# Optimization experiments

Hardware: AMD Instinct MI355X
Metric: run time of the kernel (lower is better)

The kernel has to match this reference:

```python
import jax, jax.numpy as jnp
import numpy as np

D = 256      # d_model (module-level constant in source)
H = 4        # num_heads
HD = D // H  # head dim = 64
B = 16
T = 512
STEP = 0.5   # self.step_size
NEG = -1e9
SCALE = 1.0 / np.sqrt(HD).astype(np.float32)


def _ln(x, g, b):
    m = jnp.mean(x, -1, keepdims=True)
    v = jnp.var(x, -1, keepdims=True)
    return (x - m) / jnp.sqrt(v + 1e-5) * g + b


def _forward(x, h0,
             sa_wq, sa_wk, sa_wv, sa_wo, sa_bq, sa_bk, sa_bv, sa_bo,
             f_w1, f_b1, f_w2, f_b2,
             ta_wq, ta_wk, ta_wv, ta_wo, ta_bq, ta_bk, ta_bv, ta_bo,
             tr_w1, tr_b1, tr_w2, tr_b2,
             ps_w, ps_b, sp_w, sp_b,
             ln1_g, ln1_b, ln2_g, ln2_b, ln3_g, ln3_b, ln4_g, ln4_b):
    Bz, Tz, Dz = x.shape
    # ---- causal self-attention over parallel_repr ----
    q = (x @ sa_wq + sa_bq).reshape(Bz, Tz, H, HD)
    k = (x @ sa_wk + sa_bk).reshape(Bz, Tz, H, HD)
    v = (x @ sa_wv + sa_bv).reshape(Bz, Tz, H, HD)
    scores = jnp.einsum('bqhd,bkhd->bhqk', q, k) * SCALE
    causal = jnp.tril(jnp.ones((Tz, Tz), bool))
    scores = jnp.where(causal, scores, NEG)
    attn = jnp.einsum('bhqk,bkhd->bqhd', jax.nn.softmax(scores, -1), v)
    attn = attn.reshape(Bz, Tz, Dz) @ sa_wo + sa_bo
    x = _ln(x + attn, ln1_g, ln1_b)
    # ---- FFN with sequential guidance ----
    guid = h0 @ sp_w + sp_b                      # sequential_to_parallel, [B, D]
    ffn_in = x + 0.3 * guid[:, None, :]
    ffn = jax.nn.gelu(ffn_in @ f_w1 + f_b1, approximate=False) @ f_w2 + f_b2
    x = _ln(x + ffn, ln2_g, ln2_b)
    # ---- sequential scan with growing-cache trajectory attention ----
    # past states only enter through their K/V projections, so project each
    # new state once when it is appended (same math as re-projecting the cache).
    def step(carry, inp):
        h, kbuf, vbuf = carry                    # kbuf/vbuf: [T, B, H, HD]
        t, xt = inp                              # xt: [B, D]
        qt = (xt @ ta_wq + ta_bq).reshape(Bz, H, HD)
        sc = jnp.einsum('bhd,tbhd->bht', qt, kbuf) * SCALE
        valid = (jnp.arange(Tz) < t)[None, None, :]
        ctx = jnp.einsum('bht,tbhd->bhd',
                         jax.nn.softmax(jnp.where(valid, sc, NEG), -1), vbuf)
        ctx = ctx.reshape(Bz, Dz) @ ta_wo + ta_bo
        ctx = jnp.where(t > 0, ctx, 0.0)         # torch code zeroes context at t=0
        pg = xt @ ps_w + ps_b                    # parallel_to_sequential
        comb = jnp.concatenate([xt + 0.3 * pg, ctx], -1)
        delta = jax.nn.gelu(comb @ tr_w1 + tr_b1, approximate=False) @ tr_w2 + tr_b2
        h = _ln(h + STEP * delta, ln3_g, ln3_b)
        kbuf = kbuf.at[t].set((h @ ta_wk + ta_bk).reshape(Bz, H, HD))
        vbuf = vbuf.at[t].set((h @ ta_wv + ta_bv).reshape(Bz, H, HD))
        return (h, kbuf, vbuf), None

    buf0 = jnp.zeros((Tz, Bz, H, HD), x.dtype)
    (hT, _, _), _ = jax.lax.scan(step, (h0, buf0, buf0),
                                 (jnp.arange(Tz), jnp.swapaxes(x, 0, 1)))
    return x, _ln(hT, ln4_g, ln4_b)


def setup_inputs() -> dict:
    ks = iter(jax.random.split(jax.random.key(0), 64))
    def w(*shape):
        return jax.random.normal(next(ks), shape, jnp.float32) * 0.02
    inp = {
        'x': jax.random.normal(next(ks), (B, T, D), jnp.float32),
        'h0': jax.random.normal(next(ks), (B, D), jnp.float32),
        'sa_wq': w(D, D), 'sa_wk': w(D, D), 'sa_wv': w(D, D), 'sa_wo': w(D, D),
        'sa_bq': w(D), 'sa_bk': w(D), 'sa_bv': w(D), 'sa_bo': w(D),
        'f_w1': w(D, 4 * D), 'f_b1': w(4 * D), 'f_w2': w(4 * D, D), 'f_b2': w(D),
        'ta_wq': w(D, D), 'ta_wk': w(D, D), 'ta_wv': w(D, D), 'ta_wo': w(D, D),
        'ta_bq': w(D), 'ta_bk': w(D), 'ta_bv': w(D), 'ta_bo': w(D),
        'tr_w1': w(2 * D, 2 * D), 'tr_b1': w(2 * D), 'tr_w2': w(2 * D, D), 'tr_b2': w(D),
        'ps_w': w(D, D), 'ps_b': w(D), 'sp_w': w(D, D), 'sp_b': w(D),
        'ln1_g': jnp.ones(D), 'ln1_b': jnp.zeros(D),
        'ln2_g': jnp.ones(D), 'ln2_b': jnp.zeros(D),
        'ln3_g': jnp.ones(D), 'ln3_b': jnp.zeros(D),
        'ln4_g': jnp.ones(D), 'ln4_b': jnp.zeros(D),
    }
    return inp


def reference(x, h0,
              sa_wq, sa_wk, sa_wv, sa_wo, sa_bq, sa_bk, sa_bv, sa_bo,
              f_w1, f_b1, f_w2, f_b2,
              ta_wq, ta_wk, ta_wv, ta_wo, ta_bq, ta_bk, ta_bv, ta_bo,
              tr_w1, tr_b1, tr_w2, tr_b2,
              ps_w, ps_b, sp_w, sp_b,
              ln1_g, ln1_b, ln2_g, ln2_b, ln3_g, ln3_b, ln4_g, ln4_b):
    return _forward(x, h0,
                    sa_wq, sa_wk, sa_wv, sa_wo, sa_bq, sa_bk, sa_bv, sa_bo,
                    f_w1, f_b1, f_w2, f_b2,
                    ta_wq, ta_wk, ta_wv, ta_wo, ta_bq, ta_bk, ta_bv, ta_bo,
                    tr_w1, tr_b1, tr_w2, tr_b2,
                    ps_w, ps_b, sp_w, sp_b,
                    ln1_g, ln1_b, ln2_g, ln2_b, ln3_g, ln3_b, ln4_g, ln4_b)
```

## Files before the change

### kernel.cpp

```cpp
#include <hip/hip_runtime.h>
#include <hip/hip_bf16.h>

typedef __bf16 bf16x8 __attribute__((ext_vector_type(8)));
typedef float f32x4 __attribute__((ext_vector_type(4)));

__device__ __forceinline__ float b2f(ushort u){
  union { uint u; float f; } x; x.u = ((uint)u) << 16; return x.f;
}
__device__ __forceinline__ ushort f2b(float f){
  union { float f; uint u; } x; x.f = f;
  uint r = x.u + 0x7fff + ((x.u >> 16) & 1);
  return (ushort)(r >> 16);
}
__device__ __forceinline__ uint pack_bf2(float a, float b){
  return (uint)f2b(a) | ((uint)f2b(b) << 16);
}
__device__ __forceinline__ float lo16(uint u){ union{uint a;float f;}x; x.a=u<<16; return x.f; }
__device__ __forceinline__ float hi16(uint u){ union{uint a;float f;}x; x.a=u&0xffff0000u; return x.f; }
__device__ __forceinline__ float gelu_exact(float v){
  return 0.5f * v * (1.0f + erff(v * 0.70710678118654752f));
}

union U64F2 { unsigned long long u; float2 f; };

template<int AF32, int ACT>
__global__ __launch_bounds__(256) void gemm_kernel(
    const void* __restrict__ Av, const float* __restrict__ W, int ldw,
    const float* __restrict__ bias, const float* residf,
    float* Cf, ushort* Cb,
    int M, int N, int K, float scale)
{
  __shared__ __align__(16) ushort Al[64*40];
  __shared__ __align__(16) ushort Bl[64*40];
  const int nb = N >> 6;
  const int rb = blockIdx.x / nb, cb = blockIdx.x % nb;
  const int tid = threadIdx.x;
  const int w = tid >> 6, l = tid & 63;
  f32x4 acc[4];
#pragma unroll
  for(int i=0;i<4;i++) acc[i] = (f32x4){0.f,0.f,0.f,0.f};
  const int ar = tid >> 2, ai = (tid & 3) << 3;
  const int bk = tid >> 3, bn = (tid & 7) << 3;
  for(int kb = 0; kb < K; kb += 32){
    uint4 au;
    if(AF32){
      const float* Ap = (const float*)Av + (size_t)(rb*64 + ar)*K + kb + ai;
      float4 f0 = *(const float4*)Ap;
      float4 f1 = *(const float4*)(Ap + 4);
      au.x = pack_bf2(f0.x,f0.y); au.y = pack_bf2(f0.z,f0.w);
      au.z = pack_bf2(f1.x,f1.y); au.w = pack_bf2(f1.z,f1.w);
    } else {
      au = *(const uint4*)((const ushort*)Av + (size_t)(rb*64 + ar)*K + kb + ai);
    }
    const float* Wp = W + (size_t)(kb + bk)*ldw + cb*64 + bn;
    float4 w0 = *(const float4*)Wp;
    float4 w1 = *(const float4*)(Wp + 4);
    ushort bs[8];
    bs[0]=f2b(w0.x); bs[1]=f2b(w0.y); bs[2]=f2b(w0.z); bs[3]=f2b(w0.w);
    bs[4]=f2b(w1.x); bs[5]=f2b(w1.y); bs[6]=f2b(w1.z); bs[7]=f2b(w1.w);
    __syncthreads();
    *(uint4*)&Al[ar*40 + ai] = au;
#pragma unroll
    for(int i=0;i<8;i++) Bl[(bn+i)*40 + bk] = bs[i];
    __syncthreads();
    bf16x8 af = *(const bf16x8*)&Al[(w*16 + (l&15))*40 + (l>>4)*8];
#pragma unroll
    for(int c4=0;c4<4;c4++){
      bf16x8 bfv = *(const bf16x8*)&Bl[(c4*16 + (l&15))*40 + (l>>4)*8];
      acc[c4] = __builtin_amdgcn_mfma_f32_16x16x32_bf16(af, bfv, acc[c4], 0,0,0);
    }
  }
#pragma unroll
  for(int c4=0;c4<4;c4++){
#pragma unroll
    for(int r=0;r<4;r++){
      int row = rb*64 + w*16 + (l>>4)*4 + r;
      int col = cb*64 + c4*16 + (l&15);
      size_t idx = (size_t)row*N + col;
      float vv = acc[c4][r];
      if(bias) vv += bias[col];
      vv *= scale;
      if(residf) vv += residf[idx];
      if(ACT) vv = gelu_exact(vv);
      if(Cf) Cf[idx] = vv;
      if(Cb) Cb[idx] = f2b(vv);
    }
  }
}

__global__ __launch_bounds__(256) void attn_kernel(const ushort* __restrict__ Q,
    const ushort* __restrict__ K, const ushort* __restrict__ V, ushort* __restrict__ O)
{
  __shared__ float s[16*520];
  __shared__ float kt[64*66];
  __shared__ float rowm[16], rowr[16], redx[256];
  const int bid = blockIdx.x;
  const int qb = bid & 31, h = (bid>>5)&3, b = bid>>7;
  const int tid = threadIdx.x;
  const int qi = tid >> 4, jj = tid & 15;
  const int qrow = qb*16 + qi;
  float qreg[64];
  {
    const ushort* qp = Q + ((size_t)(b*512 + qrow))*256 + h*64;
#pragma unroll
    for(int d=0; d<64; d++) qreg[d] = b2f(qp[d])*0.125f;
  }
  const int ntile = (qb*16 + 79) >> 6;
  for(int jt=0; jt<ntile; jt++){
    {
      int jr = tid >> 2, d0 = (tid & 3) << 4;
      const ushort* kp = K + ((size_t)(b*512 + jt*64 + jr))*256 + h*64 + d0;
#pragma unroll
      for(int i=0;i<16;i++) kt[jr*66 + d0 + i] = b2f(kp[i]);
    }
    __syncthreads();
#pragma unroll
    for(int jl=0;jl<4;jl++){
      int jloc = jj*4 + jl;
      int j = jt*64 + jloc;
      float a = 0.f;
#pragma unroll
      for(int d=0; d<64; d++) a += qreg[d]*kt[jloc*66 + d];
      s[qi*520 + j] = (j <= qrow) ? a : -1e30f;
    }
    __syncthreads();
  }
  const int nj = ntile*64;
  float m = -1e30f;
  for(int j=jj; j<nj; j+=16) m = fmaxf(m, s[qi*520 + j]);
  redx[jj*16 + qi] = m;
  __syncthreads();
  if(tid < 16){
    float mm = -1e30f;
#pragma unroll
    for(int k2=0;k2<16;k2++) mm = fmaxf(mm, redx[k2*16 + tid]);
    rowm[tid] = mm;
  }
  __syncthreads();
  float mrow = rowm[qi];
  float ssum = 0.f;
  for(int j=jj; j<nj; j+=16){
    float e = __expf(s[qi*520+j] - mrow);
    s[qi*520+j] = e; ssum += e;
  }
  redx[jj*16 + qi] = ssum;
  __syncthreads();
  if(tid < 16){
    float t2 = 0.f;
#pragma unroll
    for(int k2=0;k2<16;k2++) t2 += redx[k2*16 + tid];
    rowr[tid] = 1.0f/t2;
  }
  const int dd = jj;
  float acc4[4] = {0,0,0,0};
  for(int jt=0; jt<ntile; jt++){
    __syncthreads();
    {
      int jr = tid >> 2, d0 = (tid & 3) << 4;
      const ushort* vp = V + ((size_t)(b*512 + jt*64 + jr))*256 + h*64 + d0;
#pragma unroll
      for(int i=0;i<16;i++) kt[jr*66 + d0 + i] = b2f(vp[i]);
    }
    __syncthreads();
#pragma unroll
    for(int jl=0;jl<64;jl++){
      float p = s[qi*520 + jt*64 + jl];
#pragma unroll
      for(int i=0;i<4;i++) acc4[i] += p*kt[jl*66 + dd*4 + i];
    }
  }
  float rr = rowr[qi];
  ushort* op = O + ((size_t)(b*512 + qrow))*256 + h*64 + dd*4;
#pragma unroll
  for(int i=0;i<4;i++) op[i] = f2b(acc4[i]*rr);
}

__global__ __launch_bounds__(256) void ln_kernel(const float* __restrict__ in,
    const float* __restrict__ g, const float* __restrict__ be,
    float* outf, ushort* outb)
{
  int row = blockIdx.x*4 + (threadIdx.x>>6);
  int lane = threadIdx.x & 63;
  size_t idx = (size_t)row*256 + lane*4;
  float4 v = *(const float4*)(in + idx);
  float s1 = v.x+v.y+v.z+v.w;
  float s2 = v.x*v.x + v.y*v.y + v.z*v.z + v.w*v.w;
#pragma unroll
  for(int off=32; off; off>>=1){ s1 += __shfl_xor(s1,off); s2 += __shfl_xor(s2,off); }
  float mu = s1*(1.f/256.f);
  float var = s2*(1.f/256.f) - mu*mu;
  float r = rsqrtf(var + 1e-5f);
  float vals[4] = {v.x,v.y,v.z,v.w};
  float4 o4; ushort4 ob;
  float* oo = (float*)&o4; ushort* obp = (ushort*)&ob;
#pragma unroll
  for(int i=0;i<4;i++){
    int d = lane*4 + i;
    float y = (vals[i]-mu)*r*g[d] + be[d];
    oo[i] = y; obp[i] = f2b(y);
  }
  if(outf) *(float4*)(outf+idx) = o4;
  if(outb) *(ushort4*)(outb+idx) = ob;
}

__global__ void guid_kernel(const float* __restrict__ h0, const float* __restrict__ spw,
                            const float* __restrict__ spb, float* __restrict__ guid)
{
  int b = blockIdx.x, c = threadIdx.x;
  float s = spb[c];
  for(int r=0;r<256;r++) s += h0[b*256+r]*spw[r*256+c];
  guid[b*256+c] = s;
}

__global__ void ffnin_kernel(const float* __restrict__ x1, const float* __restrict__ guid,
                             ushort* __restrict__ out)
{
  size_t base = ((size_t)blockIdx.x*256 + threadIdx.x)*8;
  int row = (int)(base >> 8); int bb = row >> 9; int c = (int)(base & 255);
  float4 v0 = *(const float4*)(x1 + base);
  float4 v1 = *(const float4*)(x1 + base + 4);
  const float* gp = guid + bb*256 + c;
  const float* xs = (const float*)&v0;
  ushort o[8];
#pragma unroll
  for(int i=0;i<4;i++) o[i] = f2b(xs[i] + 0.3f*gp[i]);
  const float* xs1 = (const float*)&v1;
#pragma unroll
  for(int i=0;i<4;i++) o[4+i] = f2b(xs1[i] + 0.3f*gp[4+i]);
  *(uint4*)(out + base) = *(uint4*)o;
}

__global__ void bo_kernel(const float* __restrict__ ta_bo, const float* __restrict__ tr_w1,
                          float* __restrict__ bo_f)
{
  int c = threadIdx.x;
  float s = 0.f;
  for(int m=0;m<256;m++) s += ta_bo[m]*tr_w1[(size_t)(256+m)*512 + c];
  bo_f[c] = s;
}

__global__ __launch_bounds__(512, 1) void scan_kernel(
    const ushort* __restrict__ qtb, const ushort* __restrict__ Ubf,
    const float* __restrict__ Wf, const float* __restrict__ bo_f,
    float2* cbuf, float2* dbuf, int* flags,
    const float* __restrict__ ta_wk, const float* __restrict__ ta_wv,
    const float* __restrict__ ta_bk, const float* __restrict__ ta_bv,
    const float* __restrict__ tr_w2, const float* __restrict__ tr_b2,
    const float* __restrict__ ln3_g, const float* __restrict__ ln3_b,
    const float* __restrict__ ln4_g, const float* __restrict__ ln4_b,
    const float* __restrict__ h0, float* __restrict__ out_h)
{
  __shared__ __align__(16) float red[2][1024];
  __shared__ __align__(16) float pbuf[512];
  __shared__ __align__(16) float hbuf[256];
  __shared__ __align__(16) float ctxL[256];
  __shared__ __align__(16) float qbufS[2][64];
  __shared__ float mG[2][16], sG[2][16];
  __shared__ __align__(16) float numS[2][64];
  __shared__ float mzS[2][2];
  __shared__ float sLastP[4];
  __shared__ __align__(16) float glbuf[128];
  __shared__ int cp_same[4];
  extern __shared__ __align__(16) ushort dynL[];
  ushort* kcL = dynL;
  ushort* vcL = dynL + 512*66;

  const int tid = threadIdx.x;
  const int bid = blockIdx.x;
  const int b = bid & 15;
  const int role = bid >> 4;
  const int b4 = b*4;

  if(role < 4){
    for(int i = tid; i < 512*66; i += 512){ kcL[i] = 0; vcL[i] = 0; }
  }

  int myxcc;
  asm volatile("s_getreg_b32 %0, hwreg(HW_REG_XCC_ID)" : "=s"(myxcc));
  if(tid == 0)
    __hip_atomic_store(&flags[256 + bid], myxcc + 1, __ATOMIC_RELEASE, __HIP_MEMORY_SCOPE_AGENT);
  if(tid < 4){
    int cbid = (role < 4) ? (64 + tid*16 + b) : (tid*16 + b);
    int v;
    while((v = __hip_atomic_load(&flags[256 + cbid], __ATOMIC_ACQUIRE, __HIP_MEMORY_SCOPE_AGENT)) == 0)
      __builtin_amdgcn_s_sleep(8);
    cp_same[tid] = ((v - 1) == myxcc);
  }
  __syncthreads();
  const int anyrem = !(cp_same[0] && cp_same[1] && cp_same[2] && cp_same[3]);

  if(role < 4){
    const int hd = role;
    const int out = tid >> 2, sX = tid & 3;
    const int kvSel = out >> 6, colX = out & 63;
    const float* WX = kvSel ? ta_wv : ta_wk;
    uint wp[32];
#pragma unroll
    for(int i=0;i<32;i++){
      int r0 = 8*i + 2*sX;
      wp[i] = pack_bf2(WX[(size_t)r0*256 + hd*64 + colX],
                       WX[(size_t)(r0+1)*256 + hd*64 + colX]);
    }
    const float pbX = kvSel ? ta_bv[hd*64 + colX] : ta_bk[hd*64 + colX];
    float h4[4], b2r4[4], g34[4], b34[4];
    if(tid < 64){
#pragma unroll
      for(int c=0;c<4;c++){
        int d = 4*tid + c;
        h4[c] = h0[b*256 + d]; b2r4[c] = tr_b2[d]; g34[c] = ln3_g[d]; b34[c] = ln3_b[d];
      }
      *(float4*)&hbuf[4*tid] = *(float4*)h4;
    }
    const int j_sh = (tid >= 64) ? (tid - 64) : (448 + tid);
    const int gsh = j_sh >> 5;
    const int lsh = tid & 31;
    __syncthreads();

    ushort qpre = 0;
    if(tid >= 448) qpre = qtb[((size_t)(b*512 + 1))*256 + hd*64 + (tid - 448)];

#pragma clang loop unroll(disable)
    for(int t=0;t<512;t++){
      if(tid >= 448){
        qbufS[(t+1)&1][tid-448] = b2f(qpre)*0.125f;
        int tq = (t+2 < 512) ? (t+2) : 511;
        qpre = qtb[((size_t)(b*512 + tq))*256 + hd*64 + (tid - 448)];
      }
      if(t > 0){
        float aa0=0.f, aa1=0.f, aa2=0.f, aa3=0.f;
#pragma unroll
        for(int i=0;i<32;i+=4){
          float2 h0v = *(const float2*)&hbuf[8*i + 2*sX];
          float2 h1v = *(const float2*)&hbuf[8*(i+1) + 2*sX];
          float2 h2v = *(const float2*)&hbuf[8*(i+2) + 2*sX];
          float2 h3v = *(const float2*)&hbuf[8*(i+3) + 2*sX];
          aa0 += h0v.x*lo16(wp[i])   + h0v.y*hi16(wp[i]);
          aa1 += h1v.x*lo16(wp[i+1]) + h1v.y*hi16(wp[i+1]);
          aa2 += h2v.x*lo16(wp[i+2]) + h2v.y*hi16(wp[i+2]);
          aa3 += h3v.x*lo16(wp[i+3]) + h3v.y*hi16(wp[i+3]);
        }
        float acc = (aa0+aa1)+(aa2+aa3);
        acc += __shfl_xor(acc, 1);
        acc += __shfl_xor(acc, 2);
        float kf = acc + pbX;
        if(sX == 0){
          ushort u = f2b(kf);
          if(kvSel == 0) kcL[(t-1)*66 + colX] = u;
          else           vcL[(t-1)*66 + colX] = u;
        }
        float pv = (kvSel == 0 && sX == 0) ? qbufS[t&1][colX]*kf : 0.f;
        pv += __shfl_xor(pv, 4);
        pv += __shfl_xor(pv, 8);
        pv += __shfl_xor(pv, 16);
        pv += __shfl_xor(pv, 32);
        if(tid < 256 && (tid & 63) == 0) sLastP[tid >> 6] = pv;
        __syncthreads();
        if(tid < 64){
          const int par = t & 1;
          float sl = (sLastP[0] + sLastP[1]) + (sLastP[2] + sLastP[3]);
          float mo = mzS[par][0], Zo = mzS[par][1];
          float m = fmaxf(mo, sl);
          float so = __expf(mo - m);
          float el = __expf(sl - m);
          float Z = Zo*so + el;
          float vlast = b2f(vcL[(t-1)*66 + tid]);
          U64F2 st; st.f.x = (numS[par][tid]*so + el*vlast) / Z; st.f.y = (float)t;
          unsigned long long* cp = (unsigned long long*)&cbuf[b*256 + hd*64 + tid];
          if(!anyrem){ *cp = st.u; asm volatile("" ::: "memory"); }
          else __hip_atomic_store(cp, st.u, __ATOMIC_RELEASE, __HIP_MEMORY_SCOPE_AGENT);
        }
      }

      {
        const int par = (t+1)&1;
        float s = -3.0e38f;
        if(j_sh < t){
          const uint* kr = (const uint*)(kcL + j_sh*66);
          const float* qS = qbufS[par];
          float a0=0.f, a1=0.f, a2=0.f, a3=0.f;
#pragma unroll
          for(int w=0; w<32; w+=4){
            uint k0 = kr[w], k1 = kr[w+1], k2 = kr[w+2], k3 = kr[w+3];
            float2 q0 = *(const float2*)&qS[2*w];
            float2 q1 = *(const float2*)&qS[2*(w+1)];
            float2 q2 = *(const float2*)&qS[2*(w+2)];
            float2 q3 = *(const float2*)&qS[2*(w+3)];
            a0 += q0.x*lo16(k0) + q0.y*hi16(k0);
            a1 += q1.x*lo16(k1) + q1.y*hi16(k1);
            a2 += q2.x*lo16(k2) + q2.y*hi16(k2);
            a3 += q3.x*lo16(k3) + q3.y*hi16(k3);
          }
          s = (a0+a1)+(a2+a3);
        }
        float gm = s;
#pragma unroll
        for(int off=16; off; off>>=1) gm = fmaxf(gm, __shfl_xor(gm, off));
        float e = (j_sh < t) ? __expf(s - gm) : 0.f;
        pbuf[j_sh] = e;
        float gs = e;
#pragma unroll
        for(int off=16; off; off>>=1) gs += __shfl_xor(gs, off);
        if(lsh == 0){ mG[par][gsh] = gm; sG[par][gsh] = gs; }
        int nn = t - gsh*32; nn = nn < 0 ? 0 : (nn > 32 ? 32 : nn);
        float a0 = 0.f, a1 = 0.f;
        const uint* vbase = (const uint*)vcL;
#pragma unroll 4
        for(int i=0;i<nn;i++){
          int j2 = gsh*32 + i;
          uint vv = vbase[j2*33 + lsh];
          float p = pbuf[j2];
          a0 += p*lo16(vv); a1 += p*hi16(vv);
        }
        float2 pr; pr.x = a0; pr.y = a1;
        *(float2*)&red[par][gsh*64 + 2*lsh] = pr;
      }
      __syncthreads();
      if(tid < 64){
        const int par = (t+1)&1;
        float m0 = mG[par][0], m1 = mG[par][1];
#pragma unroll
        for(int g=2; g<16; g+=2){ m0 = fmaxf(m0, mG[par][g]); m1 = fmaxf(m1, mG[par][g+1]); }
        float mo = fmaxf(m0, m1);
        float Zo0=0.f, Zo1=0.f, nm0=0.f, nm1=0.f;
#pragma unroll
        for(int g=0; g<16; g+=2){
          float sc0 = __expf(mG[par][g] - mo);
          float sc1 = __expf(mG[par][g+1] - mo);
          Zo0 += sG[par][g]*sc0;   Zo1 += sG[par][g+1]*sc1;
          nm0 += red[par][g*64 + tid]*sc0;
          nm1 += red[par][(g+1)*64 + tid]*sc1;
        }
        numS[par][tid] = nm0 + nm1;
        if(tid == 0){ mzS[par][0] = mo; mzS[par][1] = Zo0 + Zo1; }
      }
      if(tid < 64){
        float ds[4] = {0.f,0.f,0.f,0.f};
        const float want = (float)(t+1);
        U64F2 xx[16];
        if(!anyrem){
          int ok;
          do{
            ok = 1;
#pragma unroll
            for(int i=0;i<4;i++)
#pragma unroll
              for(int c=0;c<4;c++)
                xx[i*4+c].u = *(volatile unsigned long long*)&dbuf[(b4+i)*256 + 4*tid + c];
#pragma unroll
            for(int k2=0;k2<16;k2++) ok &= (xx[k2].f.y == want);
          } while(!ok);
        } else {
          int ok;
          do{
            ok = 1;
#pragma unroll
            for(int i=0;i<4;i++)
#pragma unroll
              for(int c=0;c<4;c++){
                unsigned long long* pp = (unsigned long long*)&dbuf[(b4+i)*256 + 4*tid + c];
                xx[i*4+c].u = cp_same[i] ? *(volatile unsigned long long*)pp
                    : __hip_atomic_load(pp, __ATOMIC_RELAXED, __HIP_MEMORY_SCOPE_AGENT);
              }
#pragma unroll
            for(int k2=0;k2<16;k2++) ok &= (xx[k2].f.y == want);
            if(!ok) __builtin_amdgcn_s_sleep(1);
          } while(!ok);
        }
#pragma unroll
        for(int i=0;i<4;i++)
#pragma unroll
          for(int c=0;c<4;c++) ds[c] += xx[i*4+c].f.x;
        float v4[4]; float s1 = 0.f, s2 = 0.f;
#pragma unroll
        for(int c=0;c<4;c++){
          v4[c] = h4[c] + 0.5f*(ds[c] + b2r4[c]);
          s1 += v4[c]; s2 += v4[c]*v4[c];
        }
#pragma unroll
        for(int off=32; off; off>>=1){ s1 += __shfl_xor(s1,off); s2 += __shfl_xor(s2,off); }
        float mu = s1*(1.f/256.f);
        float qq = s2*(1.f/256.f) - mu*mu;
        float rstd = rsqrtf(qq + 1e-5f);
#pragma unroll
        for(int c=0;c<4;c++) h4[c] = (v4[c]-mu)*rstd*g34[c] + b34[c];
        *(float4*)&hbuf[4*tid] = *(float4*)h4;
      }
      __syncthreads();
    }

    if(hd == 0 && tid < 64){
      float s1 = 0.f, s2 = 0.f;
#pragma unroll
      for(int c=0;c<4;c++){ s1 += h4[c]; s2 += h4[c]*h4[c]; }
#pragma unroll
      for(int off=32; off; off>>=1){ s1 += __shfl_xor(s1,off); s2 += __shfl_xor(s2,off); }
      float mu = s1*(1.f/256.f);
      float qq = s2*(1.f/256.f) - mu*mu;
      float rstd = rsqrtf(qq + 1e-5f);
#pragma unroll
      for(int c=0;c<4;c++){
        int d = 4*tid + c;
        out_h[b*256 + d] = (h4[c]-mu)*rstd*ln4_g[d] + ln4_b[d];
      }
    }
  } else {
    const int ish = role - 4;
    const int hid = tid >> 2, sY = tid & 3;
    const int colY = ish*128 + hid;
    uint wfp[32];
#pragma unroll
    for(int i=0;i<32;i++){
      int r0 = 8*i + 2*sY;
      wfp[i] = pack_bf2(Wf[(size_t)r0*512 + colY], Wf[(size_t)(r0+1)*512 + colY]);
    }
    const int dcol = tid >> 1, s2 = tid & 1;
    uint w2p[32];
#pragma unroll
    for(int i=0;i<32;i++){
      int r0 = ish*128 + 4*i + 2*s2;
      w2p[i] = pack_bf2(tr_w2[(size_t)r0*256 + dcol], tr_w2[(size_t)(r0+1)*256 + dcol]);
    }
    const float borr = (sY==0) ? bo_f[colY] : 0.f;
    __syncthreads();

#pragma clang loop unroll(disable)
    for(int t=0;t<512;t++){
      ushort uvs = 0;
      if(sY == 0) uvs = Ubf[((size_t)(b*512 + t))*512 + colY];
      if(t > 0){
        if(tid < 256){
          const int q = tid >> 6;
          unsigned long long* sp = (unsigned long long*)&cbuf[b*256 + tid];
          U64F2 x;
          const float tf = (float)t;
          if(cp_same[q]){
            do { x.u = *(volatile unsigned long long*)sp; } while(x.f.y != tf);
          } else {
            for(;;){
              x.u = __hip_atomic_load(sp, __ATOMIC_RELAXED, __HIP_MEMORY_SCOPE_AGENT);
              if(x.f.y == tf) break;
              __builtin_amdgcn_s_sleep(1);
            }
          }
          ctxL[tid] = x.f.x;
        }
      }
      __syncthreads();
      float accf = 0.f;
      if(t > 0){
        float aa0=0.f, aa1=0.f, aa2=0.f, aa3=0.f;
#pragma unroll
        for(int i=0;i<32;i+=4){
          float2 c0 = *(const float2*)&ctxL[8*i + 2*sY];
          float2 c1 = *(const float2*)&ctxL[8*(i+1) + 2*sY];
          float2 c2 = *(const float2*)&ctxL[8*(i+2) + 2*sY];
          float2 c3 = *(const float2*)&ctxL[8*(i+3) + 2*sY];
          aa0 += c0.x*lo16(wfp[i])   + c0.y*hi16(wfp[i]);
          aa1 += c1.x*lo16(wfp[i+1]) + c1.y*hi16(wfp[i+1]);
          aa2 += c2.x*lo16(wfp[i+2]) + c2.y*hi16(wfp[i+2]);
          aa3 += c3.x*lo16(wfp[i+3]) + c3.y*hi16(wfp[i+3]);
        }
        accf = (aa0+aa1)+(aa2+aa3);
        accf += __shfl_xor(accf, 1);
        accf += __shfl_xor(accf, 2);
      }
      if(sY == 0){
        float g1 = b2f(uvs) + ((t>0) ? (borr + accf) : 0.f);
        glbuf[hid] = gelu_exact(g1);
      }
      __syncthreads();
      {
        float aa0=0.f, aa1=0.f, aa2=0.f, aa3=0.f;
#pragma unroll
        for(int i=0;i<32;i+=4){
          float2 g0 = *(const float2*)&glbuf[4*i + 2*s2];
          float2 g1v = *(const float2*)&glbuf[4*(i+1) + 2*s2];
          float2 g2 = *(const float2*)&glbuf[4*(i+2) + 2*s2];
          float2 g3 = *(const float2*)&glbuf[4*(i+3) + 2*s2];
          aa0 += g0.x*lo16(w2p[i])    + g0.y*hi16(w2p[i]);
          aa1 += g1v.x*lo16(w2p[i+1]) + g1v.y*hi16(w2p[i+1]);
          aa2 += g2.x*lo16(w2p[i+2])  + g2.y*hi16(w2p[i+2]);
          aa3 += g3.x*lo16(w2p[i+3])  + g3.y*hi16(w2p[i+3]);
        }
        float dp = (aa0+aa1)+(aa2+aa3);
        dp += __shfl_xor(dp, 1);
        if(s2 == 0){
          U64F2 st; st.f.x = dp; st.f.y = (float)(t+1);
          unsigned long long* pp = (unsigned long long*)&dbuf[(b4+ish)*256 + dcol];
          if(!anyrem){ *pp = st.u; asm volatile("" ::: "memory"); }
          else __hip_atomic_store(pp, st.u, __ATOMIC_RELEASE, __HIP_MEMORY_SCOPE_AGENT);
        }
      }
    }
  }
}

#define OFF_FLAGS ((size_t)0)
#define OFF_BOF   ((size_t)8192)
#define OFF_CBUF  ((size_t)16384)
#define OFF_DBUF  ((size_t)49152)
#define OFF_GUID  ((size_t)180224)
#define OFF_WF    ((size_t)196608)
#define OFF_Z1    ((size_t)(1u<<20))
#define OFF_Z2    ((size_t)(5u<<20))
#define OFF_Z3    ((size_t)(9u<<20))
#define OFF_Z4    ((size_t)(13u<<20))
#define OFF_M     ((size_t)(17u<<20))

#define SCAN_DYN_LDS (512*66*2*2)

extern "C" void kernel_launch(void* const* d_in, const int* in_sizes, int n_in,
                              void* d_out, int out_size, void* d_ws, size_t ws_size,
                              hipStream_t stream)
{
  const float* x     = (const float*)d_in[0];
  const float* h0    = (const float*)d_in[1];
  const float* sa_wq = (const float*)d_in[2];
  const float* sa_wk = (const float*)d_in[3];
  const float* sa_wv = (const float*)d_in[4];
  const float* sa_wo = (const float*)d_in[5];
  const float* sa_bq = (const float*)d_in[6];
  const float* sa_bk = (const float*)d_in[7];
  const float* sa_bv = (const float*)d_in[8];
  const float* sa_bo = (const float*)d_in[9];
  const float* f_w1  = (const float*)d_in[10];
  const float* f_b1  = (const float*)d_in[11];
  const float* f_w2  = (const float*)d_in[12];
  const float* f_b2  = (const float*)d_in[13];
  const float* ta_wq = (const float*)d_in[14];
  const float* ta_wk = (const float*)d_in[15];
  const float* ta_wv = (const float*)d_in[16];
  const float* ta_wo = (const float*)d_in[17];
  const float* ta_bq = (const float*)d_in[18];
  const float* ta_bk = (const float*)d_in[19];
  const float* ta_bv = (const float*)d_in[20];
  const float* ta_bo = (const float*)d_in[21];
  const float* tr_w1 = (const float*)d_in[22];
  const float* tr_b1 = (const float*)d_in[23];
  const float* tr_w2 = (const float*)d_in[24];
  const float* tr_b2 = (const float*)d_in[25];
  const float* ps_w  = (const float*)d_in[26];
  const float* ps_b  = (const float*)d_in[27];
  const float* sp_w  = (const float*)d_in[28];
  const float* sp_b  = (const float*)d_in[29];
  const float* ln1_g = (const float*)d_in[30];
  const float* ln1_b = (const float*)d_in[31];
  const float* ln2_g = (const float*)d_in[32];
  const float* ln2_b = (const float*)d_in[33];
  const float* ln3_g = (const float*)d_in[34];
  const float* ln3_b = (const float*)d_in[35];
  const float* ln4_g = (const float*)d_in[36];
  const float* ln4_b = (const float*)d_in[37];

  char* ws = (char*)d_ws;
  int*    flags = (int*)   (ws + OFF_FLAGS);
  float*  bo_f  = (float*) (ws + OFF_BOF);
  float2* cbuf  = (float2*)(ws + OFF_CBUF);
  float2* dbuf  = (float2*)(ws + OFF_DBUF);
  float*  guid  = (float*) (ws + OFF_GUID);
  float*  Wff   = (float*) (ws + OFF_WF);
  ushort* qb    = (ushort*)(ws + OFF_Z1);
  ushort* kb    = (ushort*)(ws + OFF_Z2);
  ushort* vb    = (ushort*)(ws + OFF_Z3);
  ushort* attnb = (ushort*)(ws + OFF_Z4);
  float*  x0pre = (float*) (ws + OFF_Z1);
  float*  x1f   = (float*) (ws + OFF_Z3);
  ushort* ffnb  = (ushort*)(ws + OFF_M);
  ushort* mid   = (ushort*)(ws + OFF_M + (4u<<20));
  float*  x2pre = (float*) (ws + OFF_Z1);
  ushort* abf   = (ushort*)(ws + OFF_Z4);
  ushort* qtb   = (ushort*)(ws + OFF_Z3);
  ushort* Ubf   = (ushort*)(ws + OFF_M);
  float*  outb  = (float*)d_out;
  float*  out_h = outb + (out_size - 4096);

  static int attr_done = 0;
  if(!attr_done){
    hipFuncSetAttribute((const void*)scan_kernel,
                        hipFuncAttributeMaxDynamicSharedMemorySize, SCAN_DYN_LDS);
    attr_done = 1;
  }

  hipMemsetAsync(ws, 0, OFF_GUID, stream);

  gemm_kernel<1,0><<<512, 256, 0, stream>>>(x, sa_wq, 256, sa_bq, nullptr, nullptr, qb, 8192,256,256, 1.0f);
  gemm_kernel<1,0><<<512, 256, 0, stream>>>(x, sa_wk, 256, sa_bk, nullptr, nullptr, kb, 8192,256,256, 1.0f);
  gemm_kernel<1,0><<<512, 256, 0, stream>>>(x, sa_wv, 256, sa_bv, nullptr, nullptr, vb, 8192,256,256, 1.0f);
  attn_kernel<<<2048, 256, 0, stream>>>(qb, kb, vb, attnb);
  gemm_kernel<0,0><<<512, 256, 0, stream>>>(attnb, sa_wo, 256, sa_bo, x, x0pre, nullptr, 8192,256,256, 1.0f);
  ln_kernel<<<2048, 256, 0, stream>>>(x0pre, ln1_g, ln1_b, x1f, nullptr);
  guid_kernel<<<16, 256, 0, stream>>>(h0, sp_w, sp_b, guid);
  ffnin_kernel<<<1024, 256, 0, stream>>>(x1f, guid, ffnb);
  gemm_kernel<0,1><<<1024, 256, 0, stream>>>(ffnb, f_w1, 1024, f_b1, nullptr, nullptr, mid, 8192,512,256, 1.0f);
  gemm_kernel<0,0><<<512, 256, 0, stream>>>(mid, f_w2, 256, f_b2, x1f, x2pre, nullptr, 8192,256,512, 1.0f);
  gemm_kernel<0,1><<<1024, 256, 0, stream>>>(ffnb, f_w1 + 512, 1024, f_b1 + 512, nullptr, nullptr, mid, 8192,512,256, 1.0f);
  gemm_kernel<0,0><<<512, 256, 0, stream>>>(mid, f_w2 + (size_t)512*256, 256, nullptr, x2pre, x2pre, nullptr, 8192,256,512, 1.0f);
  ln_kernel<<<2048, 256, 0, stream>>>(x2pre, ln2_g, ln2_b, outb, nullptr);

  gemm_kernel<1,0><<<512, 256, 0, stream>>>(outb, ps_w, 256, ps_b, outb, nullptr, abf, 8192,256,256, 0.3f);
  gemm_kernel<0,0><<<1024, 256, 0, stream>>>(abf, tr_w1, 512, tr_b1, nullptr, nullptr, Ubf, 8192,512,256, 1.0f);
  gemm_kernel<1,0><<<512, 256, 0, stream>>>(outb, ta_wq, 256, ta_bq, nullptr, nullptr, qtb, 8192,256,256, 1.0f);
  gemm_kernel<1,0><<<32, 256, 0, stream>>>(ta_wo, tr_w1 + (size_t)256*512, 512, nullptr, nullptr, Wff, nullptr, 256,512,256, 1.0f);
  bo_kernel<<<1, 512, 0, stream>>>(ta_bo, tr_w1, bo_f);

  scan_kernel<<<128, 512, SCAN_DYN_LDS, stream>>>(qtb, Ubf, Wff, bo_f, cbuf, dbuf, flags,
                                                  ta_wk, ta_wv, ta_bk, ta_bv, tr_w2, tr_b2,
                                                  ln3_g, ln3_b, ln4_g, ln4_b, h0, out_h);
}
```

Before: 3.530 ms.

## Overlap scan attention with state update; transpose swizzled V cache; vectorize LDS reads

Moves the per-step trajectory-attention score and P·V partial computation into the threads that were idle while the tid<64 threads do the LayerNorm state update, removing one block barrier per step. The online-softmax merge of the group partials moves to the start of the next step. The V cache is stored transposed with an XOR swizzle and K rows are padded to 72, so score and P·V loops read 128-bit vectors. Weight packing is reordered so the matvecs read float4 from LDS. The trade-off is more LDS, extra zero-initialisation, and more complex parity and indexing logic that could hide races.

```diff
diff --git a/kernel.cpp b/kernel.cpp
--- a/kernel.cpp
+++ b/kernel.cpp
@@ -263,7 +263,7 @@
   __shared__ int cp_same[4];
   extern __shared__ __align__(16) ushort dynL[];
   ushort* kcL = dynL;
-  ushort* vcL = dynL + 512*66;
+  ushort* vcT = dynL + 512*72;
 
   const int tid = threadIdx.x;
   const int bid = blockIdx.x;
@@ -272,7 +272,7 @@
   const int b4 = b*4;
 
   if(role < 4){
-    for(int i = tid; i < 512*66; i += 512){ kcL[i] = 0; vcL[i] = 0; }
+    for(int i = tid; i < 512*72 + 64*520; i += 512) dynL[i] = 0;
   }
 
   int myxcc;
@@ -296,10 +296,12 @@
     const float* WX = kvSel ? ta_wv : ta_wk;
     uint wp[32];
 #pragma unroll
-    for(int i=0;i<32;i++){
-      int r0 = 8*i + 2*sX;
-      wp[i] = pack_bf2(WX[(size_t)r0*256 + hd*64 + colX],
-                       WX[(size_t)(r0+1)*256 + hd*64 + colX]);
+    for(int i=0;i<16;i++){
+      int r0 = 16*i + 4*sX;
+      wp[2*i]   = pack_bf2(WX[(size_t)r0*256 + hd*64 + colX],
+                           WX[(size_t)(r0+1)*256 + hd*64 + colX]);
+      wp[2*i+1] = pack_bf2(WX[(size_t)(r0+2)*256 + hd*64 + colX],
+                           WX[(size_t)(r0+3)*256 + hd*64 + colX]);
     }
     const float pbX = kvSel ? ta_bv[hd*64 + colX] : ta_bk[hd*64 + colX];
     float h4[4], b2r4[4], g34[4], b34[4];
@@ -311,9 +313,16 @@
       }
       *(float4*)&hbuf[4*tid] = *(float4*)h4;
     }
-    const int j_sh = (tid >= 64) ? (tid - 64) : (448 + tid);
-    const int gsh = j_sh >> 5;
-    const int lsh = tid & 31;
+    const int j1 = tid - 64;
+    const int g1 = j1 >> 5;
+    const int l32 = tid & 31;
+    const int jB = tid + 320;
+    const int gB = 14 + ((tid - 128) >> 5);
+    for(int i=tid;i<2048;i+=512) red[i>>10][i&1023] = 0.f;
+    if(tid<32){ mG[tid>>4][tid&15] = -3.0e38f; sG[tid>>4][tid&15] = 0.f; }
+    if(tid>=448) pbuf[tid] = 0.f;
+    if(tid<128) numS[tid>>6][tid&63] = 0.f;
+    if(tid<4){ mzS[tid>>1][tid&1] = (tid&1) ? 0.f : -3.0e38f; }
     __syncthreads();
 
     ushort qpre = 0;
@@ -321,34 +330,52 @@
 
 #pragma clang loop unroll(disable)
     for(int t=0;t<512;t++){
+      const int parN = (t+1)&1;
+      const int parC = t&1;
       if(tid >= 448){
-        qbufS[(t+1)&1][tid-448] = b2f(qpre)*0.125f;
+        qbufS[parN][tid-448] = b2f(qpre)*0.125f;
         int tq = (t+2 < 512) ? (t+2) : 511;
         qpre = qtb[((size_t)(b*512 + tq))*256 + hd*64 + (tid - 448)];
       }
+      if(tid >= 64 && tid < 128){
+        const int d = tid - 64;
+        float m0 = mG[parC][0], m1 = mG[parC][1];
+#pragma unroll
+        for(int g=2; g<16; g+=2){ m0 = fmaxf(m0, mG[parC][g]); m1 = fmaxf(m1, mG[parC][g+1]); }
+        float mo = fmaxf(m0, m1);
+        float Zo0=0.f, Zo1=0.f, nm0=0.f, nm1=0.f;
+#pragma unroll
+        for(int g=0; g<16; g+=2){
+          float sc0 = __expf(mG[parC][g] - mo);
+          float sc1 = __expf(mG[parC][g+1] - mo);
+          Zo0 += sG[parC][g]*sc0;   Zo1 += sG[parC][g+1]*sc1;
+          nm0 += red[parC][g*64 + d]*sc0;
+          nm1 += red[parC][(g+1)*64 + d]*sc1;
+        }
+        numS[parC][d] = nm0 + nm1;
+        if(d == 0){ mzS[parC][0] = mo; mzS[parC][1] = Zo0 + Zo1; }
+      }
       if(t > 0){
-        float aa0=0.f, aa1=0.f, aa2=0.f, aa3=0.f;
-#pragma unroll
-        for(int i=0;i<32;i+=4){
-          float2 h0v = *(const float2*)&hbuf[8*i + 2*sX];
-          float2 h1v = *(const float2*)&hbuf[8*(i+1) + 2*sX];
-          float2 h2v = *(const float2*)&hbuf[8*(i+2) + 2*sX];
-          float2 h3v = *(const float2*)&hbuf[8*(i+3) + 2*sX];
-          aa0 += h0v.x*lo16(wp[i])   + h0v.y*hi16(wp[i]);
-          aa1 += h1v.x*lo16(wp[i+1]) + h1v.y*hi16(wp[i+1]);
-          aa2 += h2v.x*lo16(wp[i+2]) + h2v.y*hi16(wp[i+2]);
-          aa3 += h3v.x*lo16(wp[i+3]) + h3v.y*hi16(wp[i+3]);
-        }
-        float acc = (aa0+aa1)+(aa2+aa3);
+        float aa[4] = {0.f,0.f,0.f,0.f};
+#pragma unroll
+        for(int i=0;i<16;i++){
+          float4 hv = *(const float4*)&hbuf[16*i + 4*sX];
+          aa[i&3] += hv.x*lo16(wp[2*i])   + hv.y*hi16(wp[2*i])
+                   + hv.z*lo16(wp[2*i+1]) + hv.w*hi16(wp[2*i+1]);
+        }
+        float acc = (aa[0]+aa[1])+(aa[2]+aa[3]);
         acc += __shfl_xor(acc, 1);
         acc += __shfl_xor(acc, 2);
         float kf = acc + pbX;
         if(sX == 0){
           ushort u = f2b(kf);
-          if(kvSel == 0) kcL[(t-1)*66 + colX] = u;
-          else           vcL[(t-1)*66 + colX] = u;
-        }
-        float pv = (kvSel == 0 && sX == 0) ? qbufS[t&1][colX]*kf : 0.f;
+          if(kvSel == 0) kcL[(t-1)*72 + colX] = u;
+          else {
+            int cc = (t-1)>>3, sw = (colX>>1)&7;
+            vcT[colX*520 + ((cc^sw)<<3) + ((t-1)&7)] = u;
+          }
+        }
+        float pv = (kvSel == 0 && sX == 0) ? qbufS[parC][colX]*kf : 0.f;
         pv += __shfl_xor(pv, 4);
         pv += __shfl_xor(pv, 8);
         pv += __shfl_xor(pv, 16);
@@ -356,83 +383,21 @@
         if(tid < 256 && (tid & 63) == 0) sLastP[tid >> 6] = pv;
         __syncthreads();
         if(tid < 64){
-          const int par = t & 1;
           float sl = (sLastP[0] + sLastP[1]) + (sLastP[2] + sLastP[3]);
-          float mo = mzS[par][0], Zo = mzS[par][1];
+          float mo = mzS[parC][0], Zo = mzS[parC][1];
           float m = fmaxf(mo, sl);
           float so = __expf(mo - m);
           float el = __expf(sl - m);
           float Z = Zo*so + el;
-          float vlast = b2f(vcL[(t-1)*66 + tid]);
-          U64F2 st; st.f.x = (numS[par][tid]*so + el*vlast) / Z; st.f.y = (float)t;
+          int cc = (t-1)>>3, sw = (tid>>1)&7;
+          float vlast = b2f(vcT[tid*520 + ((cc^sw)<<3) + ((t-1)&7)]);
+          U64F2 st; st.f.x = (numS[parC][tid]*so + el*vlast) / Z; st.f.y = (float)t;
           unsigned long long* cp = (unsigned long long*)&cbuf[b*256 + hd*64 + tid];
           if(!anyrem){ *cp = st.u; asm volatile("" ::: "memory"); }
           else __hip_atomic_store(cp, st.u, __ATOMIC_RELEASE, __HIP_MEMORY_SCOPE_AGENT);
         }
       }
 
-      {
-        const int par = (t+1)&1;
-        float s = -3.0e38f;
-        if(j_sh < t){
-          const uint* kr = (const uint*)(kcL + j_sh*66);
-          const float* qS = qbufS[par];
-          float a0=0.f, a1=0.f, a2=0.f, a3=0.f;
-#pragma unroll
-          for(int w=0; w<32; w+=4){
-            uint k0 = kr[w], k1 = kr[w+1], k2 = kr[w+2], k3 = kr[w+3];
-            float2 q0 = *(const float2*)&qS[2*w];
-            float2 q1 = *(const float2*)&qS[2*(w+1)];
-            float2 q2 = *(const float2*)&qS[2*(w+2)];
-            float2 q3 = *(const float2*)&qS[2*(w+3)];
-            a0 += q0.x*lo16(k0) + q0.y*hi16(k0);
-            a1 += q1.x*lo16(k1) + q1.y*hi16(k1);
-            a2 += q2.x*lo16(k2) + q2.y*hi16(k2);
-            a3 += q3.x*lo16(k3) + q3.y*hi16(k3);
-          }
-          s = (a0+a1)+(a2+a3);
-        }
-        float gm = s;
-#pragma unroll
-        for(int off=16; off; off>>=1) gm = fmaxf(gm, __shfl_xor(gm, off));
-        float e = (j_sh < t) ? __expf(s - gm) : 0.f;
-        pbuf[j_sh] = e;
-        float gs = e;
-#pragma unroll
-        for(int off=16; off; off>>=1) gs += __shfl_xor(gs, off);
-        if(lsh == 0){ mG[par][gsh] = gm; sG[par][gsh] = gs; }
-        int nn = t - gsh*32; nn = nn < 0 ? 0 : (nn > 32 ? 32 : nn);
-        float a0 = 0.f, a1 = 0.f;
-        const uint* vbase = (const uint*)vcL;
-#pragma unroll 4
-        for(int i=0;i<nn;i++){
-          int j2 = gsh*32 + i;
-          uint vv = vbase[j2*33 + lsh];
-          float p = pbuf[j2];
-          a0 += p*lo16(vv); a1 += p*hi16(vv);
-        }
-        float2 pr; pr.x = a0; pr.y = a1;
-        *(float2*)&red[par][gsh*64 + 2*lsh] = pr;
-      }
-      __syncthreads();
-      if(tid < 64){
-        const int par = (t+1)&1;
-        float m0 = mG[par][0], m1 = mG[par][1];
-#pragma unroll
-        for(int g=2; g<16; g+=2){ m0 = fmaxf(m0, mG[par][g]); m1 = fmaxf(m1, mG[par][g+1]); }
-        float mo = fmaxf(m0, m1);
-        float Zo0=0.f, Zo1=0.f, nm0=0.f, nm1=0.f;
-#pragma unroll
-        for(int g=0; g<16; g+=2){
-          float sc0 = __expf(mG[par][g] - mo);
-          float sc1 = __expf(mG[par][g+1] - mo);
-          Zo0 += sG[par][g]*sc0;   Zo1 += sG[par][g+1]*sc1;
-          nm0 += red[par][g*64 + tid]*sc0;
-          nm1 += red[par][(g+1)*64 + tid]*sc1;
-        }
-        numS[par][tid] = nm0 + nm1;
-        if(tid == 0){ mzS[par][0] = mo; mzS[par][1] = Zo0 + Zo1; }
-      }
       if(tid < 64){
         float ds[4] = {0.f,0.f,0.f,0.f};
         const float want = (float)(t+1);
@@ -484,6 +449,101 @@
 #pragma unroll
         for(int c=0;c<4;c++) h4[c] = (v4[c]-mu)*rstd*g34[c] + b34[c];
         *(float4*)&hbuf[4*tid] = *(float4*)h4;
+      } else {
+        {
+          float s = -3.0e38f;
+          if(j1 < t){
+            const uint4* kr4 = (const uint4*)(kcL + j1*72);
+            const float4* q4 = (const float4*)qbufS[parN];
+            float a0=0.f,a1=0.f,a2=0.f,a3=0.f;
+#pragma unroll
+            for(int c=0;c<8;c++){
+              uint4 kk = kr4[c];
+              float4 qa = q4[2*c], qb2 = q4[2*c+1];
+              a0 += qa.x*lo16(kk.x) + qa.y*hi16(kk.x);
+              a1 += qa.z*lo16(kk.y) + qa.w*hi16(kk.y);
+              a2 += qb2.x*lo16(kk.z) + qb2.y*hi16(kk.z);
+              a3 += qb2.z*lo16(kk.w) + qb2.w*hi16(kk.w);
+            }
+            s = (a0+a1)+(a2+a3);
+          }
+          float gm = s;
+#pragma unroll
+          for(int off=16; off; off>>=1) gm = fmaxf(gm, __shfl_xor(gm, off));
+          float e = (j1 < t) ? __expf(s - gm) : 0.f;
+          pbuf[j1] = e;
+          float gs = e;
+#pragma unroll
+          for(int off=16; off; off>>=1) gs += __shfl_xor(gs, off);
+          if(l32 == 0){ mG[parN][g1] = gm; sG[parN][g1] = gs; }
+        }
+        if(tid >= 128 && tid < 192 && t > 448){
+          float s = -3.0e38f;
+          if(jB < t){
+            const uint4* kr4 = (const uint4*)(kcL + jB*72);
+            const float4* q4 = (const float4*)qbufS[parN];
+            float a0=0.f,a1=0.f,a2=0.f,a3=0.f;
+#pragma unroll
+            for(int c=0;c<8;c++){
+              uint4 kk = kr4[c];
+              float4 qa = q4[2*c], qb2 = q4[2*c+1];
+              a0 += qa.x*lo16(kk.x) + qa.y*hi16(kk.x);
+              a1 += qa.z*lo16(kk.y) + qa.w*hi16(kk.y);
+              a2 += qb2.x*lo16(kk.z) + qb2.y*hi16(kk.z);
+              a3 += qb2.z*lo16(kk.w) + qb2.w*hi16(kk.w);
+            }
+            s = (a0+a1)+(a2+a3);
+          }
+          float gm = s;
+#pragma unroll
+          for(int off=16; off; off>>=1) gm = fmaxf(gm, __shfl_xor(gm, off));
+          float e = (jB < t) ? __expf(s - gm) : 0.f;
+          pbuf[jB] = e;
+          float gs = e;
+#pragma unroll
+          for(int off=16; off; off>>=1) gs += __shfl_xor(gs, off);
+          if(l32 == 0){ mG[parN][gB] = gm; sG[parN][gB] = gs; }
+        }
+        {
+          const int sw = l32 & 7;
+          const ushort* r0p = vcT + (2*l32)*520;
+          const ushort* r1p = vcT + (2*l32+1)*520;
+          const float4* p4 = (const float4*)(pbuf + g1*32);
+          float a0=0.f, a1=0.f;
+#pragma unroll
+          for(int q=0;q<4;q++){
+            int cc = g1*4 + q;
+            uint4 v0 = *(const uint4*)(r0p + ((cc^sw)<<3));
+            uint4 v1 = *(const uint4*)(r1p + ((cc^sw)<<3));
+            float4 pA = p4[2*q], pB = p4[2*q+1];
+            a0 += pA.x*lo16(v0.x)+pA.y*hi16(v0.x)+pA.z*lo16(v0.y)+pA.w*hi16(v0.y)
+                + pB.x*lo16(v0.z)+pB.y*hi16(v0.z)+pB.z*lo16(v0.w)+pB.w*hi16(v0.w);
+            a1 += pA.x*lo16(v1.x)+pA.y*hi16(v1.x)+pA.z*lo16(v1.y)+pA.w*hi16(v1.y)
+                + pB.x*lo16(v1.z)+pB.y*hi16(v1.z)+pB.z*lo16(v1.w)+pB.w*hi16(v1.w);
+          }
+          float2 pr; pr.x = a0; pr.y = a1;
+          *(float2*)&red[parN][g1*64 + 2*l32] = pr;
+        }
+        if(tid >= 128 && tid < 192 && t > 448){
+          const int sw = l32 & 7;
+          const ushort* r0p = vcT + (2*l32)*520;
+          const ushort* r1p = vcT + (2*l32+1)*520;
+          const float4* p4 = (const float4*)(pbuf + gB*32);
+          float a0=0.f, a1=0.f;
+#pragma unroll
+          for(int q=0;q<4;q++){
+            int cc = gB*4 + q;
+            uint4 v0 = *(const uint4*)(r0p + ((cc^sw)<<3));
+            uint4 v1 = *(const uint4*)(r1p + ((cc^sw)<<3));
+            float4 pA = p4[2*q], pB = p4[2*q+1];
+            a0 += pA.x*lo16(v0.x)+pA.y*hi16(v0.x)+pA.z*lo16(v0.y)+pA.w*hi16(v0.y)
+                + pB.x*lo16(v0.z)+pB.y*hi16(v0.z)+pB.z*lo16(v0.w)+pB.w*hi16(v0.w);
+            a1 += pA.x*lo16(v1.x)+pA.y*hi16(v1.x)+pA.z*lo16(v1.y)+pA.w*hi16(v1.y)
+                + pB.x*lo16(v1.z)+pB.y*hi16(v1.z)+pB.z*lo16(v1.w)+pB.w*hi16(v1.w);
+          }
+          float2 pr; pr.x = a0; pr.y = a1;
+          *(float2*)&red[parN][gB*64 + 2*l32] = pr;
+        }
       }
       __syncthreads();
     }
@@ -509,16 +569,18 @@
     const int colY = ish*128 + hid;
     uint wfp[32];
 #pragma unroll
-    for(int i=0;i<32;i++){
-      int r0 = 8*i + 2*sY;
-      wfp[i] = pack_bf2(Wf[(size_t)r0*512 + colY], Wf[(size_t)(r0+1)*512 + colY]);
+    for(int i=0;i<16;i++){
+      int r0 = 16*i + 4*sY;
+      wfp[2*i]   = pack_bf2(Wf[(size_t)r0*512 + colY], Wf[(size_t)(r0+1)*512 + colY]);
+      wfp[2*i+1] = pack_bf2(Wf[(size_t)(r0+2)*512 + colY], Wf[(size_t)(r0+3)*512 + colY]);
     }
     const int dcol = tid >> 1, s2 = tid & 1;
     uint w2p[32];
 #pragma unroll
-    for(int i=0;i<32;i++){
-      int r0 = ish*128 + 4*i + 2*s2;
-      w2p[i] = pack_bf2(tr_w2[(size_t)r0*256 + dcol], tr_w2[(size_t)(r0+1)*256 + dcol]);
+    for(int i=0;i<16;i++){
+      int r0 = ish*128 + 8*i + 4*s2;
+      w2p[2*i]   = pack_bf2(tr_w2[(size_t)r0*256 + dcol], tr_w2[(size_t)(r0+1)*256 + dcol]);
+      w2p[2*i+1] = pack_bf2(tr_w2[(size_t)(r0+2)*256 + dcol], tr_w2[(size_t)(r0+3)*256 + dcol]);
     }
     const float borr = (sY==0) ? bo_f[colY] : 0.f;
     __syncthreads();
@@ -548,19 +610,14 @@
       __syncthreads();
       float accf = 0.f;
       if(t > 0){
-        float aa0=0.f, aa1=0.f, aa2=0.f, aa3=0.f;
-#pragma unroll
-        for(int i=0;i<32;i+=4){
-          float2 c0 = *(const float2*)&ctxL[8*i + 2*sY];
-          float2 c1 = *(const float2*)&ctxL[8*(i+1) + 2*sY];
-          float2 c2 = *(const float2*)&ctxL[8*(i+2) + 2*sY];
-          float2 c3 = *(const float2*)&ctxL[8*(i+3) + 2*sY];
-          aa0 += c0.x*lo16(wfp[i])   + c0.y*hi16(wfp[i]);
-          aa1 += c1.x*lo16(wfp[i+1]) + c1.y*hi16(wfp[i+1]);
-          aa2 += c2.x*lo16(wfp[i+2]) + c2.y*hi16(wfp[i+2]);
-          aa3 += c3.x*lo16(wfp[i+3]) + c3.y*hi16(wfp[i+3]);
-        }
-        accf = (aa0+aa1)+(aa2+aa3);
+        float aa[4] = {0.f,0.f,0.f,0.f};
+#pragma unroll
+        for(int i=0;i<16;i++){
+          float4 cv = *(const float4*)&ctxL[16*i + 4*sY];
+          aa[i&3] += cv.x*lo16(wfp[2*i])   + cv.y*hi16(wfp[2*i])
+                   + cv.z*lo16(wfp[2*i+1]) + cv.w*hi16(wfp[2*i+1]);
+        }
+        accf = (aa[0]+aa[1])+(aa[2]+aa[3]);
         accf += __shfl_xor(accf, 1);
         accf += __shfl_xor(accf, 2);
       }
@@ -570,19 +627,14 @@
       }
       __syncthreads();
       {
-        float aa0=0.f, aa1=0.f, aa2=0.f, aa3=0.f;
-#pragma unroll
-        for(int i=0;i<32;i+=4){
-          float2 g0 = *(const float2*)&glbuf[4*i + 2*s2];
-          float2 g1v = *(const float2*)&glbuf[4*(i+1) + 2*s2];
-          float2 g2 = *(const float2*)&glbuf[4*(i+2) + 2*s2];
-          float2 g3 = *(const float2*)&glbuf[4*(i+3) + 2*s2];
-          aa0 += g0.x*lo16(w2p[i])    + g0.y*hi16(w2p[i]);
-          aa1 += g1v.x*lo16(w2p[i+1]) + g1v.y*hi16(w2p[i+1]);
-          aa2 += g2.x*lo16(w2p[i+2])  + g2.y*hi16(w2p[i+2]);
-          aa3 += g3.x*lo16(w2p[i+3])  + g3.y*hi16(w2p[i+3]);
-        }
-        float dp = (aa0+aa1)+(aa2+aa3);
+        float aa[4] = {0.f,0.f,0.f,0.f};
+#pragma unroll
+        for(int i=0;i<16;i++){
+          float4 gv = *(const float4*)&glbuf[8*i + 4*s2];
+          aa[i&3] += gv.x*lo16(w2p[2*i])   + gv.y*hi16(w2p[2*i])
+                   + gv.z*lo16(w2p[2*i+1]) + gv.w*hi16(w2p[2*i+1]);
+        }
+        float dp = (aa[0]+aa[1])+(aa[2]+aa[3]);
         dp += __shfl_xor(dp, 1);
         if(s2 == 0){
           U64F2 st; st.f.x = dp; st.f.y = (float)(t+1);
@@ -607,7 +659,7 @@
 #define OFF_Z4    ((size_t)(13u<<20))
 #define OFF_M     ((size_t)(17u<<20))
 
-#define SCAN_DYN_LDS (512*66*2*2)
+#define SCAN_DYN_LDS ((512*72 + 64*520)*2)
 
 extern "C" void kernel_launch(void* const* d_in, const int* in_sizes, int n_in,
                               void* d_out, int out_size, void* d_ws, size_t ws_size,
```

Measured after the change: 3.551 ms. Within noise of the previous version (+0.6%).
